# Kernel tuning notes

Measured on AMD Instinct MI355X. Metric: run time of the kernel, lower is better.

## Reference

```python
import jax, jax.numpy as jnp
import numpy as np

C = 10.0
EMBEDDING_DIM = 128


def setup_inputs() -> dict:
    key = jax.random.key(0)
    k1, k2 = jax.random.split(key)
    B, P, D, N = 128, 128, 128, 4096
    mh_attn_out = jax.random.normal(k1, (B, P, D), dtype=jnp.float32)
    single_head_key = jax.random.normal(k2, (B, D, N), dtype=jnp.float32)
    mask = jnp.zeros((B, P, N), dtype=jnp.float32)  # additive mask (0 or -inf)
    return {"mh_attn_out": mh_attn_out, "single_head_key": single_head_key, "mask": mask}


def reference(mh_attn_out, single_head_key, mask):
    # score: [B, P, N]
    score = jnp.einsum('bpd,bdn->bpn', mh_attn_out, single_head_key)
    score_scaled = score / jnp.sqrt(jnp.float32(EMBEDDING_DIM))
    score_clipped = C * jnp.tanh(score_scaled)
    score_masked = score_clipped + mask
    probs = jax.nn.softmax(score_masked, axis=-1)
    return probs
```

## Files before the change

### kernel.cpp

```cpp
#include <hip/hip_runtime.h>
#include <math.h>

constexpr int BB = 128;
constexpr int PP = 128;
constexpr int DD = 128;
constexpr int NN = 4096;
constexpr float kC = 10.0f;
constexpr float k2InvSqrtD = 0.1767766952966369f;

constexpr int NTHR = 512;
constexpr int TEL = 272;

typedef float f32x4 __attribute__((ext_vector_type(4)));
typedef _Float16 f16x4 __attribute__((ext_vector_type(4)));
typedef _Float16 f16x8 __attribute__((ext_vector_type(8)));

__device__ __forceinline__ void st_nt_f4(float* p, float4 s) {
    f32x4 v = {s.x, s.y, s.z, s.w};
    __builtin_nontemporal_store(v, (f32x4*)p);
}

__device__ __forceinline__ f16x4 tr_read(unsigned addr) {
    f16x4 r;
    asm volatile("ds_read_b64_tr_b16 %0, %1" : "=v"(r) : "v"(addr));
    return r;
}

__device__ __forceinline__ float clip1(float s, float m) {
    const float e2 = __expf(s * k2InvSqrtD);
    const float r = __builtin_amdgcn_rcpf(e2 + 1.0f);
    return fmaf(-2.0f * kC, r, kC) + m;
}

__global__ __launch_bounds__(NTHR, 4)
void score_kernel(const float* __restrict__ A,
                  const float* __restrict__ K,
                  const float* __restrict__ M,
                  float* __restrict__ O,
                  float* __restrict__ ws) {
    __shared__ _Float16 Khi[32 * TEL];
    __shared__ _Float16 Klo[32 * TEL];

    const int l = blockIdx.x;
    const int b = l >> 5;
    const int ntb = l & 31;
    const int n_base = ntb * 128;

    const int tid = (int)threadIdx.x;
    const int lane = tid & 63;
    const int wid = tid >> 6;
    const int col = lane & 15;
    const int g = lane >> 4;
    const int kbase = 4 * g;

    const float* Arow = A + (size_t)(b * PP + wid * 16 + col) * DD;
    f16x8 ah[4], al[4];
    #pragma unroll
    for (int kb = 0; kb < 4; ++kb) {
        #pragma unroll
        for (int j = 0; j < 8; ++j) {
            const int d = kb * 32 + kbase + (j & 3) + 16 * (j >> 2);
            const float x = Arow[d];
            const _Float16 h = (_Float16)x;
            ah[kb][j] = h;
            al[kb][j] = (_Float16)(x - (float)h);
        }
    }

    const size_t mrow0 = (size_t)(b * PP + wid * 16 + kbase) * NN + n_base + col;
    const unsigned khi0 = (unsigned)(uintptr_t)&Khi[0] + (unsigned)lane * 8u;
    const unsigned klo0 = (unsigned)(uintptr_t)&Klo[0] + (unsigned)lane * 8u;

    const float* Kg = K + (size_t)b * DD * NN + n_base;
    const int nl4 = (tid & 15) * 4;
    const int d0 = tid >> 4;
    const int el0 = ((d0 >> 4) * 4 + (nl4 >> 4)) * TEL + (d0 & 15) * 16 + (nl4 & 12);

    float rsum[4] = {0.f, 0.f, 0.f, 0.f};

    #pragma unroll
    for (int half = 0; half < 2; ++half) {
        if (half) __syncthreads();

        #pragma unroll
        for (int i = 0; i < 4; ++i) {
            const float4 v = *(const float4*)(Kg + (size_t)(d0 + 32 * i) * NN
                                              + half * 64 + nl4);
            const float xs[4] = {v.x, v.y, v.z, v.w};
            f16x4 h, lo;
            #pragma unroll
            for (int e = 0; e < 4; ++e) {
                const _Float16 hh = (_Float16)xs[e];
                h[e] = hh;
                lo[e] = (_Float16)(xs[e] - (float)hh);
            }
            const int el = el0 + i * 8 * TEL;
            *(f16x4*)&Khi[el] = h;
            *(f16x4*)&Klo[el] = lo;
        }
        __syncthreads();

        #pragma unroll
        for (int nt2 = 0; nt2 < 4; ++nt2) {
            const int nt = half * 4 + nt2;

            f32x4 acc = {0.f, 0.f, 0.f, 0.f};
            #pragma unroll
            for (int kb = 0; kb < 4; ++kb) {
                const unsigned t0 = (unsigned)(((2 * kb) * 4 + nt2) * 544);
                const f16x4 bh0 = tr_read(khi0 + t0);
                const f16x4 bh1 = tr_read(khi0 + t0 + 4u * 544u);
                const f16x4 bl0 = tr_read(klo0 + t0);
                const f16x4 bl1 = tr_read(klo0 + t0 + 4u * 544u);
                asm volatile("s_waitcnt lgkmcnt(0)" ::: "memory");
                __builtin_amdgcn_sched_barrier(0);
                const f16x8 bh = __builtin_shufflevector(bh0, bh1, 0, 1, 2, 3, 4, 5, 6, 7);
                const f16x8 bl = __builtin_shufflevector(bl0, bl1, 0, 1, 2, 3, 4, 5, 6, 7);
                acc = __builtin_amdgcn_mfma_f32_16x16x32_f16(ah[kb], bh, acc, 0, 0, 0);
                acc = __builtin_amdgcn_mfma_f32_16x16x32_f16(ah[kb], bl, acc, 0, 0, 0);
                acc = __builtin_amdgcn_mfma_f32_16x16x32_f16(al[kb], bh, acc, 0, 0, 0);
            }

            #pragma unroll
            for (int j = 0; j < 4; ++j) {
                const size_t off = mrow0 + (size_t)j * NN + nt * 16;
                const float e = __expf(clip1(acc[j], M[off]));
                O[off] = e;
                rsum[j] += e;
            }
        }
    }

    #pragma unroll
    for (int j = 0; j < 4; ++j) {
        float s = rsum[j];
        s += __shfl_xor(s, 1);
        s += __shfl_xor(s, 2);
        s += __shfl_xor(s, 4);
        s += __shfl_xor(s, 8);
        rsum[j] = s;
    }
    if (col == 0) {
        #pragma unroll
        for (int j = 0; j < 4; ++j)
            ws[(size_t)(b * PP + wid * 16 + kbase + j) * 32 + ntb] = rsum[j];
    }
}

__global__ __launch_bounds__(256, 4)
void scale_kernel(float* __restrict__ O, const float* __restrict__ ws) {
    const int gtid = blockIdx.x * 256 + (int)threadIdx.x;
    const int row = gtid >> 5;
    const int seg = gtid & 31;

    const float* w = ws + (size_t)row * 32;
    float s = 0.f;
    #pragma unroll
    for (int i = 0; i < 8; ++i) {
        const float4 v = *(const float4*)(w + i * 4);
        s += (v.x + v.y) + (v.z + v.w);
    }
    const float inv = __builtin_amdgcn_rcpf(s);

    float4* R = (float4*)(O + (size_t)row * NN);
    #pragma unroll 8
    for (int i = 0; i < 32; ++i) {
        const int idx = i * 32 + seg;
        float4 v = R[idx];
        v.x *= inv; v.y *= inv; v.z *= inv; v.w *= inv;
        st_nt_f4((float*)&R[idx], v);
    }
}

extern "C" void kernel_launch(void* const* d_in, const int* in_sizes, int n_in,
                              void* d_out, int out_size, void* d_ws, size_t ws_size,
                              hipStream_t stream) {
    const float* A = (const float*)d_in[0];
    const float* K = (const float*)d_in[1];
    const float* M = (const float*)d_in[2];
    float* O = (float*)d_out;
    float* ws = (float*)d_ws;

    score_kernel<<<dim3(BB * 32), dim3(NTHR), 0, stream>>>(A, K, M, O, ws);
    scale_kernel<<<dim3(2048), dim3(256), 0, stream>>>(O, ws);
}
```

Baseline: 318.3 us.

## Transpose MFMA output so each lane writes float4 rows and prefetch mask

Swaps the A and B operands of the MFMA so each lane holds four consecutive N-columns of one P-row. Mask loads and output stores become float4 vector accesses instead of scalar strided ones. The mask is prefetched two tiles ahead, and the row-sum reduction drops to two cross-group shuffles. Launch bounds are relaxed from 4 to 2 blocks per CU, which frees registers for the prefetch but may lower occupancy.

```diff
diff --git a/kernel.cpp b/kernel.cpp
--- a/kernel.cpp
+++ b/kernel.cpp
@@ -32,7 +32,7 @@
     return fmaf(-2.0f * kC, r, kC) + m;
 }
 
-__global__ __launch_bounds__(NTHR, 4)
+__global__ __launch_bounds__(NTHR, 2)
 void score_kernel(const float* __restrict__ A,
                   const float* __restrict__ K,
                   const float* __restrict__ M,
@@ -67,7 +67,7 @@
         }
     }
 
-    const size_t mrow0 = (size_t)(b * PP + wid * 16 + kbase) * NN + n_base + col;
+    const size_t prow0 = (size_t)(b * PP + wid * 16 + col) * NN + n_base + 4 * g;
     const unsigned khi0 = (unsigned)(uintptr_t)&Khi[0] + (unsigned)lane * 8u;
     const unsigned klo0 = (unsigned)(uintptr_t)&Klo[0] + (unsigned)lane * 8u;
 
@@ -76,7 +76,10 @@
     const int d0 = tid >> 4;
     const int el0 = ((d0 >> 4) * 4 + (nl4 >> 4)) * TEL + (d0 & 15) * 16 + (nl4 & 12);
 
-    float rsum[4] = {0.f, 0.f, 0.f, 0.f};
+    float rsum = 0.f;
+
+    float4 mv = *(const float4*)(M + prow0);
+    float4 mvn = *(const float4*)(M + prow0 + 16);
 
     #pragma unroll
     for (int half = 0; half < 2; ++half) {
@@ -116,35 +119,32 @@
                 __builtin_amdgcn_sched_barrier(0);
                 const f16x8 bh = __builtin_shufflevector(bh0, bh1, 0, 1, 2, 3, 4, 5, 6, 7);
                 const f16x8 bl = __builtin_shufflevector(bl0, bl1, 0, 1, 2, 3, 4, 5, 6, 7);
-                acc = __builtin_amdgcn_mfma_f32_16x16x32_f16(ah[kb], bh, acc, 0, 0, 0);
-                acc = __builtin_amdgcn_mfma_f32_16x16x32_f16(ah[kb], bl, acc, 0, 0, 0);
-                acc = __builtin_amdgcn_mfma_f32_16x16x32_f16(al[kb], bh, acc, 0, 0, 0);
+                acc = __builtin_amdgcn_mfma_f32_16x16x32_f16(bh, ah[kb], acc, 0, 0, 0);
+                acc = __builtin_amdgcn_mfma_f32_16x16x32_f16(bl, ah[kb], acc, 0, 0, 0);
+                acc = __builtin_amdgcn_mfma_f32_16x16x32_f16(bh, al[kb], acc, 0, 0, 0);
             }
 
-            #pragma unroll
-            for (int j = 0; j < 4; ++j) {
-                const size_t off = mrow0 + (size_t)j * NN + nt * 16;
-                const float e = __expf(clip1(acc[j], M[off]));
-                O[off] = e;
-                rsum[j] += e;
+            {
+                const size_t off = prow0 + (size_t)nt * 16;
+                float4 e;
+                e.x = __expf(clip1(acc[0], mv.x));
+                e.y = __expf(clip1(acc[1], mv.y));
+                e.z = __expf(clip1(acc[2], mv.z));
+                e.w = __expf(clip1(acc[3], mv.w));
+                *(float4*)(O + off) = e;
+                rsum += (e.x + e.y) + (e.z + e.w);
             }
+
+            mv = mvn;
+            if (nt + 2 < 8)
+                mvn = *(const float4*)(M + prow0 + (size_t)(nt + 2) * 16);
         }
     }
 
-    #pragma unroll
-    for (int j = 0; j < 4; ++j) {
-        float s = rsum[j];
-        s += __shfl_xor(s, 1);
-        s += __shfl_xor(s, 2);
-        s += __shfl_xor(s, 4);
-        s += __shfl_xor(s, 8);
-        rsum[j] = s;
-    }
-    if (col == 0) {
-        #pragma unroll
-        for (int j = 0; j < 4; ++j)
-            ws[(size_t)(b * PP + wid * 16 + kbase + j) * 32 + ntb] = rsum[j];
-    }
+    rsum += __shfl_xor(rsum, 16);
+    rsum += __shfl_xor(rsum, 32);
+    if (g == 0)
+        ws[(size_t)(b * PP + wid * 16 + col) * 32 + ntb] = rsum;
 }
 
 __global__ __launch_bounds__(256, 4)
```

After: 274.9 us. -13.6%, faster.
